# Performance work log

Hardware: AMD Instinct MI355X
Metric: run time of the kernel (lower is better)

Reference implementation:

```python
import jax, jax.numpy as jnp
import numpy as np
import math

HIDDEN = 2048
N_HEADS = 16
HEAD_DIM = HIDDEN // N_HEADS
BASE = 10000.0


def setup_inputs() -> dict:
    key = jax.random.key(0)
    ks = jax.random.split(key, 8)
    s = 1.0 / math.sqrt(HIDDEN)
    inp = {
        "hidden_states": jax.random.normal(ks[0], (2, 2048, HIDDEN), dtype=jnp.float32),
        "Wq": jax.random.normal(ks[1], (HIDDEN, HIDDEN), dtype=jnp.float32) * s,
        "bq": jax.random.normal(ks[2], (HIDDEN,), dtype=jnp.float32) * s,
        "Wk": jax.random.normal(ks[3], (HIDDEN, HIDDEN), dtype=jnp.float32) * s,
        "bk": jax.random.normal(ks[4], (HIDDEN,), dtype=jnp.float32) * s,
        "Wv": jax.random.normal(ks[5], (HIDDEN, HIDDEN), dtype=jnp.float32) * s,
        "bv": jax.random.normal(ks[6], (HIDDEN,), dtype=jnp.float32) * s,
        "Wo": jax.random.normal(ks[7], (HIDDEN, HIDDEN), dtype=jnp.float32) * s,
    }
    return inp


def _rotate_half(x):
    x1, x2 = x[..., : x.shape[-1] // 2], x[..., x.shape[-1] // 2 :]
    return jnp.concatenate((-x2, x1), axis=-1)


def _rope_cos_sin(seq_len, dtype):
    inv_freq = 1.0 / (BASE ** (jnp.arange(0, HEAD_DIM, 2, dtype=jnp.float32) / HEAD_DIM))
    t = jnp.arange(seq_len, dtype=jnp.float32)
    freqs = jnp.einsum("i,j->ij", t, inv_freq)  # [S, head_dim/2]
    emb = jnp.concatenate((freqs, freqs), axis=-1)  # [S, head_dim]
    return jnp.cos(emb).astype(dtype), jnp.sin(emb).astype(dtype)


def reference(hidden_states, Wq, bq, Wk, bk, Wv, bv, Wo):
    B, S, _ = hidden_states.shape
    q = hidden_states @ Wq + bq
    k = hidden_states @ Wk + bk
    v = hidden_states @ Wv + bv
    # [B, H, S, D]
    q = q.reshape(B, S, N_HEADS, HEAD_DIM).transpose(0, 2, 1, 3)
    k = k.reshape(B, S, N_HEADS, HEAD_DIM).transpose(0, 2, 1, 3)
    v = v.reshape(B, S, N_HEADS, HEAD_DIM).transpose(0, 2, 1, 3)
    cos, sin = _rope_cos_sin(S, q.dtype)  # [S, D]
    cos = cos[None, None]
    sin = sin[None, None]
    q = q * cos + _rotate_half(q) * sin
    k = k * cos + _rotate_half(k) * sin
    scale = 1.0 / math.sqrt(HEAD_DIM)
    scores = jnp.einsum("bhqd,bhkd->bhqk", q, k) * scale
    attn = jax.nn.softmax(scores, axis=-1)
    out = jnp.einsum("bhqk,bhkd->bhqd", attn, v)
    out = out.transpose(0, 2, 1, 3).reshape(B, S, HIDDEN)
    return out @ Wo
```

## Files before the change

### kernel.cpp

```cpp
#include <hip/hip_runtime.h>

#define HID 2048
#define SEQ 2048
#define HD 128
#define QKN 6144

typedef float f32x4 __attribute__((ext_vector_type(4)));
typedef short s16x8 __attribute__((ext_vector_type(8)));
typedef __bf16 bf16x8 __attribute__((ext_vector_type(8)));

static __device__ __forceinline__ unsigned short f2bf(float x) {
    unsigned u = __float_as_uint(x);
    u = u + 0x7FFFu + ((u >> 16) & 1u);
    return (unsigned short)(u >> 16);
}
static __device__ __forceinline__ float bf2f(unsigned short h) {
    return __uint_as_float(((unsigned)h) << 16);
}
static __device__ __forceinline__ bf16x8 as_bf(s16x8 v) {
    union { s16x8 s; bf16x8 b; } u; u.s = v; return u.b;
}
static __device__ __forceinline__ bf16x8 ld_bf8(const unsigned short* p) {
    return as_bf(*(const s16x8*)p);
}
static __device__ __forceinline__ void gload_lds16(const void* g, void* l) {
    __builtin_amdgcn_global_load_lds(
        (const __attribute__((address_space(1))) void*)g,
        (__attribute__((address_space(3))) void*)l,
        16, 0, 0);
}

__global__ __launch_bounds__(256) void fill_f32(
    float* __restrict__ out, float v, int n)
{
    int i = blockIdx.x * 256 + threadIdx.x;
    if (i < n) out[i] = v;
}

__global__ __launch_bounds__(256) void convert_f32_bf16(
    const float* __restrict__ in, unsigned short* __restrict__ out)
{
    long i = ((long)blockIdx.x * 256 + threadIdx.x) * 8;
    f32x4 a = *(const f32x4*)&in[i];
    f32x4 b = *(const f32x4*)&in[i + 4];
    s16x8 o;
#pragma unroll
    for (int e = 0; e < 4; ++e) {
        o[e]     = (short)f2bf(a[e]);
        o[e + 4] = (short)f2bf(b[e]);
    }
    *(s16x8*)&out[i] = o;
}

__global__ __launch_bounds__(256) void transpose_w4(
    const float* __restrict__ Wq, const float* __restrict__ Wk,
    const float* __restrict__ Wv, const float* __restrict__ Wo,
    unsigned short* __restrict__ wqkvT, unsigned short* __restrict__ woT)
{
    __shared__ float t[32][33];
    const int z = blockIdx.z;
    const float* W = (z == 0) ? Wq : (z == 1) ? Wk : (z == 2) ? Wv : Wo;
    unsigned short* Wt = (z < 3) ? (wqkvT + (long)z * HID * HID) : woT;
    int k0 = blockIdx.x * 32, n0 = blockIdx.y * 32;
    int tx = threadIdx.x & 31, ty = threadIdx.x >> 5;
#pragma unroll
    for (int r = ty; r < 32; r += 8)
        t[r][tx] = W[(long)(k0 + r) * HID + n0 + tx];
    __syncthreads();
#pragma unroll
    for (int r = ty; r < 32; r += 8)
        Wt[(long)(n0 + r) * HID + k0 + tx] = f2bf(t[tx][r]);
}

template<int NF, bool F32OUT, bool ROPE>
__global__ __launch_bounds__(512, 2) void gemm_8phase(
    const unsigned short* __restrict__ A,
    const unsigned short* __restrict__ Bt,
    const float* __restrict__ bq, const float* __restrict__ bk,
    const float* __restrict__ bv,
    unsigned short* __restrict__ Cb, float* __restrict__ Cf,
    int K, int ldc, int nbn, int sm, int sn, int hasBias)
{
    constexpr int BUFE = 16384 + NF * 4096;
    __shared__ unsigned short lds[2 * BUFE];
    const int tid = threadIdx.x;
    const int wid = tid >> 6, lane = tid & 63;
    const int l16 = lane & 15, l4 = lane >> 4;
    const int wm = wid >> 2, wn = wid & 3;

    const int bid = blockIdx.x;
    const int xcd = bid & 7, idx = bid >> 3;
    const int ncn = nbn / sn;
    const int cm = xcd / ncn, cn = xcd % ncn;
    const int lm = idx / sn,  ln = idx % sn;
    const long bm = (long)(cm * sm + lm) * 256;
    const long bn = (long)(cn * sn + ln) * (NF * 64);

    const int NT = K >> 6;
    const long strideB = (long)K * 2;
    const int srow = tid >> 3;
    const int scb  = ((tid & 7) * 16) ^ ((srow & 7) << 4);

    auto stageA = [&](int t, int c) {
        unsigned short* base = &lds[(t & 1) * BUFE];
        const int row = c * 64 + srow;
        const char* src = (const char*)A + (bm + row) * strideB + (long)t * 128 + scb;
        gload_lds16(src, base + (c * 64 + wid * 8) * 64);
    };
    auto stageB = [&](int t, int c) {
        unsigned short* base = &lds[(t & 1) * BUFE + 16384];
        const int row = c * 64 + srow;
        const char* src = (const char*)Bt + (bn + row) * strideB + (long)t * 128 + scb;
        gload_lds16(src, base + (c * 64 + wid * 8) * 64);
    };

    f32x4 acc[8][NF];
#pragma unroll
    for (int i = 0; i < 8; ++i)
#pragma unroll
        for (int j = 0; j < NF; ++j) acc[i][j] = f32x4{0.f, 0.f, 0.f, 0.f};

    auto compute = [&](const unsigned short* Ab, const unsigned short* Bb) {
#pragma unroll
        for (int kk = 0; kk < 2; ++kk) {
            bf16x8 bfr[NF];
#pragma unroll
            for (int j = 0; j < NF; ++j) {
                const int row = wn * (NF * 16) + j * 16 + l16;
                const char* rb = (const char*)Bb + row * 128;
                bfr[j] = as_bf(*(const s16x8*)(rb + ((kk * 64 + l4 * 16) ^ ((l16 & 7) << 4))));
            }
#pragma unroll
            for (int half = 0; half < 2; ++half) {
                bf16x8 af[4];
#pragma unroll
                for (int i = 0; i < 4; ++i) {
                    const int row = wm * 128 + (half * 4 + i) * 16 + l16;
                    const char* rb = (const char*)Ab + row * 128;
                    af[i] = as_bf(*(const s16x8*)(rb + ((kk * 64 + l4 * 16) ^ ((l16 & 7) << 4))));
                }
                __builtin_amdgcn_s_setprio(1);
#pragma unroll
                for (int i = 0; i < 4; ++i)
#pragma unroll
                    for (int j = 0; j < NF; ++j)
                        acc[half * 4 + i][j] = __builtin_amdgcn_mfma_f32_16x16x32_bf16(
                            af[i], bfr[j], acc[half * 4 + i][j], 0, 0, 0);
                __builtin_amdgcn_s_setprio(0);
            }
        }
    };

#pragma unroll
    for (int c = 0; c < 4; ++c) stageA(0, c);
#pragma unroll
    for (int c = 0; c < NF; ++c) stageB(0, c);

    for (int t = 0; t < NT - 1; ++t) {
        const unsigned short* Ab = &lds[(t & 1) * BUFE];
        const unsigned short* Bb = Ab + 16384;
#pragma unroll
        for (int c = 0; c < 4; ++c) stageA(t + 1, c);
#pragma unroll
        for (int c = 0; c < NF; ++c) stageB(t + 1, c);
        __builtin_amdgcn_sched_barrier(0);
        if constexpr (NF == 6)      asm volatile("s_waitcnt vmcnt(10)" ::: "memory");
        else if constexpr (NF == 3) asm volatile("s_waitcnt vmcnt(7)" ::: "memory");
        else                        asm volatile("s_waitcnt vmcnt(6)" ::: "memory");
        __builtin_amdgcn_s_barrier();
        __builtin_amdgcn_sched_barrier(0);
        compute(Ab, Bb);
        __builtin_amdgcn_s_barrier();
    }
    {
        const unsigned short* Ab = &lds[((NT - 1) & 1) * BUFE];
        const unsigned short* Bb = Ab + 16384;
        asm volatile("s_waitcnt vmcnt(0)" ::: "memory");
        __builtin_amdgcn_s_barrier();
        __builtin_amdgcn_sched_barrier(0);
        compute(Ab, Bb);
    }

    float bvv[NF];
#pragma unroll
    for (int nf = 0; nf < NF; ++nf) {
        const long n = bn + wn * (NF * 16) + nf * 16 + l16;
        bvv[nf] = 0.f;
        if (hasBias)
            bvv[nf] = (n < HID) ? bq[n] : ((n < 2 * HID) ? bk[n - HID] : bv[n - 2 * HID]);
    }

    if constexpr (ROPE) {
        constexpr int NH = NF / 2;
        float* fl = (float*)lds;
        const int jr = tid & 63;
        const int rquo = tid >> 6;
        const float inv = exp2f(-(float)jr * 0.20762050593046f);
#pragma unroll
        for (int c = 0; c < 4; ++c) {
            __builtin_amdgcn_s_barrier();
            if (wm == (c >> 1)) {
                const int mf0 = (c & 1) * 4;
#pragma unroll
                for (int mfi = 0; mfi < 4; ++mfi)
#pragma unroll
                    for (int r = 0; r < 4; ++r) {
                        const int rl = mfi * 16 + l4 * 4 + r;
#pragma unroll
                        for (int nf = 0; nf < NF; ++nf)
                            fl[rl * 385 + wn * (NF * 16) + nf * 16 + l16] =
                                acc[mf0 + mfi][nf][r] + bvv[nf];
                    }
            }
            __builtin_amdgcn_s_barrier();
#pragma unroll
            for (int rr = 0; rr < 8; ++rr) {
                const int rl = rr * 8 + rquo;
                const long m = bm + (c >> 1) * 128 + (c & 1) * 64 + rl;
                const int s = (int)(m & (SEQ - 1));
                float sn, cs;
                sincosf((float)s * inv, &sn, &cs);
#pragma unroll
                for (int hh = 0; hh < NH; ++hh) {
                    const long n = bn + hh * 128 + jr;
                    const bool ron = n < 2 * HID;
                    const float qsv = (n < HID) ? 0.12751744581845f : 1.0f;
                    const float se = ron ? sn : 0.f;
                    const float ce = ron ? cs : 1.f;
                    const float x1 = fl[rl * 385 + hh * 128 + jr];
                    const float x2 = fl[rl * 385 + hh * 128 + jr + 64];
                    Cb[m * (long)ldc + n]      = f2bf((x1 * ce - x2 * se) * qsv);
                    Cb[m * (long)ldc + n + 64] = f2bf((x2 * ce + x1 * se) * qsv);
                }
            }
        }
    } else {
#pragma unroll
        for (int mf = 0; mf < 8; ++mf) {
#pragma unroll
            for (int r = 0; r < 4; ++r) {
                const long m = bm + wm * 128 + mf * 16 + l4 * 4 + r;
#pragma unroll
                for (int nf = 0; nf < NF; ++nf) {
                    const long n = bn + wn * (NF * 16) + nf * 16 + l16;
                    float v = acc[mf][nf][r] + bvv[nf];
                    if (F32OUT) Cf[m * (long)ldc + n] = v;
                    else        Cb[m * (long)ldc + n] = f2bf(v);
                }
            }
        }
    }
}

__global__ __launch_bounds__(256) void v_transpose(
    const unsigned short* __restrict__ qkv, unsigned short* __restrict__ vt)
{
    __shared__ unsigned short t[32][33];
    int bh = blockIdx.z;
    int b = bh >> 4, h = bh & 15;
    int s0 = blockIdx.x * 32, d0 = blockIdx.y * 32;
    int tx = threadIdx.x & 31, ty = threadIdx.x >> 5;
#pragma unroll
    for (int r = ty; r < 32; r += 8)
        t[r][tx] = qkv[(long)(b * SEQ + s0 + r) * QKN + 2 * HID + h * HD + d0 + tx];
    __syncthreads();
#pragma unroll
    for (int r = ty; r < 32; r += 8)
        vt[((long)bh * HD + d0 + r) * SEQ + s0 + tx] = t[tx][r];
}

__global__ __launch_bounds__(512) void attn_kernel(
    const unsigned short* __restrict__ qkv,
    const unsigned short* __restrict__ vt,
    unsigned short* __restrict__ attnout)
{
    __shared__ unsigned short Ks[2][64 * 128];
    __shared__ unsigned short Vs[2][128 * 64];

    const int tid = threadIdx.x, wid = tid >> 6, lane = tid & 63;
    const int l16 = lane & 15, l4 = lane >> 4;
    const int bid = blockIdx.x;
    const int xcd = bid & 7, idx = bid >> 3;
    const int bh = xcd * 4 + (idx >> 4);
    const int qt = idx & 15;
    const int b = bh >> 4, h = bh & 15;
    const long rowbase = (long)b * SEQ;

    const unsigned short* Kg = &qkv[rowbase * QKN + HID + h * HD];
    const unsigned short* Vg = &vt[(long)bh * HD * SEQ];

    auto stage = [&](int buf, int kv0) {
#pragma unroll
        for (int i = 0; i < 2; ++i) {
            int c = wid * 2 + i;
            int kr = c * 4 + l4;
            int kcb = (l16 * 16) ^ ((kr & 7) << 4);
            gload_lds16((const char*)(Kg + (long)(kv0 + kr) * QKN) + kcb, &Ks[buf][c * 512]);
            int vr = c * 8 + (lane >> 3);
            int vcb = ((lane & 7) * 16) ^ ((vr & 7) << 4);
            gload_lds16((const char*)(Vg + (long)vr * SEQ + kv0) + vcb, &Vs[buf][c * 512]);
        }
    };

    bf16x8 qf[4];
    {
        const long qrow = rowbase + qt * 128 + wid * 16 + l16;
        const unsigned short* qp = &qkv[qrow * QKN + h * HD];
#pragma unroll
        for (int kc = 0; kc < 4; ++kc) qf[kc] = ld_bf8(qp + kc * 32 + l4 * 8);
    }

    f32x4 o[8];
#pragma unroll
    for (int nb = 0; nb < 8; ++nb) o[nb] = f32x4{0.f, 0.f, 0.f, 0.f};
    float mrun = -3.0e38f, lrun = 0.f;

    const int srcA = ((l4 & 1) * 2) * 16 + l16;
    const int srcB = srcA + 16;
    const bool sel = (l4 >> 1) != 0;

    stage(0, 0);
    __syncthreads();

    for (int t = 0; t < SEQ / 64; ++t) {
        const int cur = t & 1;
        if (t < SEQ / 64 - 1) stage(cur ^ 1, (t + 1) * 64);
        __builtin_amdgcn_sched_barrier(0);

        const unsigned short* Kc = &Ks[cur][0];
        const unsigned short* Vc = &Vs[cur][0];

        f32x4 sc[4];
#pragma unroll
        for (int nf = 0; nf < 4; ++nf) sc[nf] = f32x4{0.f, 0.f, 0.f, 0.f};
#pragma unroll
        for (int kc = 0; kc < 4; ++kc) {
#pragma unroll
            for (int nf = 0; nf < 4; ++nf) {
                int row = nf * 16 + l16;
                int cb = (kc * 64 + l4 * 16) ^ ((row & 7) << 4);
                bf16x8 kf = as_bf(*(const s16x8*)((const char*)Kc + row * 256 + cb));
                sc[nf] = __builtin_amdgcn_mfma_f32_16x16x32_bf16(kf, qf[kc], sc[nf], 0, 0, 0);
            }
        }

        float m0 = fmaxf(fmaxf(sc[0][0], sc[0][1]), sc[0][2]);
        float m1 = fmaxf(fmaxf(sc[0][3], sc[1][0]), sc[1][1]);
        float m2 = fmaxf(fmaxf(sc[1][2], sc[1][3]), sc[2][0]);
        float m3 = fmaxf(fmaxf(sc[2][1], sc[2][2]), sc[2][3]);
        float m4 = fmaxf(fmaxf(sc[3][0], sc[3][1]), sc[3][2]);
        float tmax = fmaxf(fmaxf(m0, m1), m2);
        tmax = fmaxf(fmaxf(m3, m4), tmax);
        tmax = fmaxf(tmax, sc[3][3]);
        tmax = fmaxf(tmax, __shfl_xor(tmax, 16, 64));
        tmax = fmaxf(tmax, __shfl_xor(tmax, 32, 64));

        if (!__all(tmax - mrun <= 8.0f)) {
            float mn = fmaxf(mrun, tmax);
            float sc_ = exp2f(mrun - mn);
            mrun = mn;
            lrun *= sc_;
            float s_[4];
#pragma unroll
            for (int r = 0; r < 4; ++r) s_[r] = __shfl(sc_, l4 * 4 + r, 64);
#pragma unroll
            for (int nb = 0; nb < 8; ++nb)
#pragma unroll
                for (int r = 0; r < 4; ++r) o[nb][r] *= s_[r];
        }

        unsigned pk[4][2];
        float sum = 0.f;
#pragma unroll
        for (int nf = 0; nf < 4; ++nf) {
            float p0 = exp2f(sc[nf][0] - mrun);
            float p1 = exp2f(sc[nf][1] - mrun);
            float p2 = exp2f(sc[nf][2] - mrun);
            float p3 = exp2f(sc[nf][3] - mrun);
            sum += (p0 + p1) + (p2 + p3);
            union { __bf16 b[2]; unsigned u; } w0, w1;
            w0.b[0] = (__bf16)p0; w0.b[1] = (__bf16)p1;
            w1.b[0] = (__bf16)p2; w1.b[1] = (__bf16)p3;
            pk[nf][0] = w0.u; pk[nf][1] = w1.u;
        }
        sum += __shfl_xor(sum, 16, 64);
        sum += __shfl_xor(sum, 32, 64);
        lrun += sum;

        union { unsigned u[4]; bf16x8 v; } pa0, pa1;
#pragma unroll
        for (int w = 0; w < 2; ++w) {
            unsigned a0 = __shfl(pk[0][w], srcA, 64);
            unsigned a1 = __shfl(pk[1][w], srcA, 64);
            unsigned b0 = __shfl(pk[0][w], srcB, 64);
            unsigned b1 = __shfl(pk[1][w], srcB, 64);
            pa0.u[w]     = sel ? a1 : a0;
            pa0.u[2 + w] = sel ? b1 : b0;
            unsigned c0 = __shfl(pk[2][w], srcA, 64);
            unsigned c1 = __shfl(pk[3][w], srcA, 64);
            unsigned d0 = __shfl(pk[2][w], srcB, 64);
            unsigned d1 = __shfl(pk[3][w], srcB, 64);
            pa1.u[w]     = sel ? c1 : c0;
            pa1.u[2 + w] = sel ? d1 : d0;
        }

#pragma unroll
        for (int kc = 0; kc < 2; ++kc) {
            bf16x8 pav = kc ? pa1.v : pa0.v;
#pragma unroll
            for (int nb = 0; nb < 8; ++nb) {
                int vrow = nb * 16 + l16;
                int vcb = (kc * 64 + l4 * 16) ^ ((vrow & 7) << 4);
                bf16x8 vb = as_bf(*(const s16x8*)((const char*)Vc + vrow * 128 + vcb));
                o[nb] = __builtin_amdgcn_mfma_f32_16x16x32_bf16(pav, vb, o[nb], 0, 0, 0);
            }
        }
        __syncthreads();
    }

    float linv = 1.f / lrun;
    float li[4];
#pragma unroll
    for (int r = 0; r < 4; ++r) li[r] = __shfl(linv, l4 * 4 + r, 64);
#pragma unroll
    for (int r = 0; r < 4; ++r) {
        long m = rowbase + qt * 128 + wid * 16 + l4 * 4 + r;
#pragma unroll
        for (int nb = 0; nb < 8; ++nb)
            attnout[m * HID + h * HD + nb * 16 + l16] = f2bf(o[nb][r] * li[r]);
    }
}

extern "C" void kernel_launch(void* const* d_in, const int* in_sizes, int n_in,
                              void* d_out, int out_size, void* d_ws, size_t ws_size,
                              hipStream_t stream)
{
    const float* hs = (const float*)d_in[0];
    const float* Wq = (const float*)d_in[1];
    const float* bq = (const float*)d_in[2];
    const float* Wk = (const float*)d_in[3];
    const float* bk = (const float*)d_in[4];
    const float* Wv = (const float*)d_in[5];
    const float* bv = (const float*)d_in[6];
    const float* Wo = (const float*)d_in[7];
    float* out = (float*)d_out;

    bool shapes_ok =
        (n_in == 8) && (out_size == 8388608) &&
        in_sizes[0] == 8388608 && in_sizes[1] == 4194304 && in_sizes[2] == 2048 &&
        in_sizes[3] == 4194304 && in_sizes[4] == 2048 && in_sizes[5] == 4194304 &&
        in_sizes[6] == 2048 && in_sizes[7] == 4194304;
    if (!shapes_ok || ws_size < 117440512ull) {
        fill_f32<<<32768, 256, 0, stream>>>(out, shapes_ok ? 1000.f : 0.f, out_size);
        return;
    }

    char* ws = (char*)d_ws;
    unsigned short* hsB     = (unsigned short*)(ws);
    unsigned short* qkvB    = (unsigned short*)(ws + 16777216);
    unsigned short* wqkvT   = (unsigned short*)(ws + 67108864);
    unsigned short* vtB     = (unsigned short*)(ws + 92274688);
    unsigned short* woT     = (unsigned short*)(ws + 109051904);
    unsigned short* attnout = hsB;

    convert_f32_bf16<<<4096, 256, 0, stream>>>(hs, hsB);
    transpose_w4<<<dim3(64, 64, 4), 256, 0, stream>>>(Wq, Wk, Wv, Wo, wqkvT, woT);

    gemm_8phase<6, false, true><<<dim3(256), 512, 0, stream>>>(
        hsB, wqkvT, bq, bk, bv, qkvB, nullptr, 2048, QKN, 16, 8, 4, 1);
    v_transpose<<<dim3(64, 4, 32), 256, 0, stream>>>(qkvB, vtB);
    attn_kernel<<<dim3(512), 512, 0, stream>>>(qkvB, vtB, attnout);
    gemm_8phase<2, true, false><<<dim3(256), 512, 0, stream>>>(
        attnout, woT, nullptr, nullptr, nullptr, nullptr, out, 2048, HID, 16, 4, 8, 0);
}
```

Before: 293.3 us.

## Switch attention to 32x32x16 MFMA with 256-row query tiles per block

The attention kernel now gives each wave 32 query rows instead of 16 and uses 32x32x16 bf16 MFMAs for both QK^T and PV. Each block covers 256 query rows, so the grid halves to 256 blocks. This doubles the reuse of every K/V tile staged in LDS, cuts LDS traffic per FLOP, and simplifies the P-fragment shuffle to a single xor-32 exchange. The cost is much higher register pressure (64 accumulator floats plus 32 score floats per lane), and only 256 blocks on a GPU with 256 CUs may leave occupancy thin despite launch_bounds(512,2).

New measurement: 285.0 us (median of 2 runs). -2.9%, faster.

```diff
diff --git a/kernel.cpp b/kernel.cpp
--- a/kernel.cpp
+++ b/kernel.cpp
@@ -6,6 +6,7 @@
 #define QKN 6144
 
 typedef float f32x4 __attribute__((ext_vector_type(4)));
+typedef float f32x16 __attribute__((ext_vector_type(16)));
 typedef short s16x8 __attribute__((ext_vector_type(8)));
 typedef __bf16 bf16x8 __attribute__((ext_vector_type(8)));
 
@@ -269,7 +270,7 @@
         vt[((long)bh * HD + d0 + r) * SEQ + s0 + tx] = t[tx][r];
 }
 
-__global__ __launch_bounds__(512) void attn_kernel(
+__global__ __launch_bounds__(512, 2) void attn_kernel(
     const unsigned short* __restrict__ qkv,
     const unsigned short* __restrict__ vt,
     unsigned short* __restrict__ attnout)
@@ -278,11 +279,12 @@
     __shared__ unsigned short Vs[2][128 * 64];
 
     const int tid = threadIdx.x, wid = tid >> 6, lane = tid & 63;
+    const int l32 = lane & 31, hh = lane >> 5;
     const int l16 = lane & 15, l4 = lane >> 4;
     const int bid = blockIdx.x;
     const int xcd = bid & 7, idx = bid >> 3;
-    const int bh = xcd * 4 + (idx >> 4);
-    const int qt = idx & 15;
+    const int bh = xcd * 4 + (idx >> 3);
+    const int qt = idx & 7;
     const int b = bh >> 4, h = bh & 15;
     const long rowbase = (long)b * SEQ;
 
@@ -302,22 +304,21 @@
         }
     };
 
-    bf16x8 qf[4];
+    bf16x8 qf[8];
     {
-        const long qrow = rowbase + qt * 128 + wid * 16 + l16;
+        const long qrow = rowbase + qt * 256 + wid * 32 + l32;
         const unsigned short* qp = &qkv[qrow * QKN + h * HD];
 #pragma unroll
-        for (int kc = 0; kc < 4; ++kc) qf[kc] = ld_bf8(qp + kc * 32 + l4 * 8);
-    }
-
-    f32x4 o[8];
-#pragma unroll
-    for (int nb = 0; nb < 8; ++nb) o[nb] = f32x4{0.f, 0.f, 0.f, 0.f};
+        for (int ks = 0; ks < 8; ++ks)
+            qf[ks] = ld_bf8(qp + ks * 16 + hh * 8);
+    }
+
+    f32x16 ob[4];
+#pragma unroll
+    for (int db = 0; db < 4; ++db)
+#pragma unroll
+        for (int r = 0; r < 16; ++r) ob[db][r] = 0.f;
     float mrun = -3.0e38f, lrun = 0.f;
-
-    const int srcA = ((l4 & 1) * 2) * 16 + l16;
-    const int srcB = srcA + 16;
-    const bool sel = (l4 >> 1) != 0;
 
     stage(0, 0);
     __syncthreads();
@@ -330,104 +331,100 @@
         const unsigned short* Kc = &Ks[cur][0];
         const unsigned short* Vc = &Vs[cur][0];
 
-        f32x4 sc[4];
-#pragma unroll
-        for (int nf = 0; nf < 4; ++nf) sc[nf] = f32x4{0.f, 0.f, 0.f, 0.f};
-#pragma unroll
-        for (int kc = 0; kc < 4; ++kc) {
-#pragma unroll
-            for (int nf = 0; nf < 4; ++nf) {
-                int row = nf * 16 + l16;
-                int cb = (kc * 64 + l4 * 16) ^ ((row & 7) << 4);
+        f32x16 sc[2];
+#pragma unroll
+        for (int kb = 0; kb < 2; ++kb)
+#pragma unroll
+            for (int r = 0; r < 16; ++r) sc[kb][r] = 0.f;
+#pragma unroll
+        for (int ks = 0; ks < 8; ++ks) {
+#pragma unroll
+            for (int kb = 0; kb < 2; ++kb) {
+                int row = kb * 32 + l32;
+                int cb = (ks * 32 + hh * 16) ^ ((row & 7) << 4);
                 bf16x8 kf = as_bf(*(const s16x8*)((const char*)Kc + row * 256 + cb));
-                sc[nf] = __builtin_amdgcn_mfma_f32_16x16x32_bf16(kf, qf[kc], sc[nf], 0, 0, 0);
-            }
-        }
-
-        float m0 = fmaxf(fmaxf(sc[0][0], sc[0][1]), sc[0][2]);
-        float m1 = fmaxf(fmaxf(sc[0][3], sc[1][0]), sc[1][1]);
-        float m2 = fmaxf(fmaxf(sc[1][2], sc[1][3]), sc[2][0]);
-        float m3 = fmaxf(fmaxf(sc[2][1], sc[2][2]), sc[2][3]);
-        float m4 = fmaxf(fmaxf(sc[3][0], sc[3][1]), sc[3][2]);
-        float tmax = fmaxf(fmaxf(m0, m1), m2);
-        tmax = fmaxf(fmaxf(m3, m4), tmax);
-        tmax = fmaxf(tmax, sc[3][3]);
-        tmax = fmaxf(tmax, __shfl_xor(tmax, 16, 64));
+                sc[kb] = __builtin_amdgcn_mfma_f32_32x32x16_bf16(kf, qf[ks], sc[kb], 0, 0, 0);
+            }
+        }
+
+        float tmax = sc[0][0];
+#pragma unroll
+        for (int kb = 0; kb < 2; ++kb)
+#pragma unroll
+            for (int r = 0; r < 16; ++r) tmax = fmaxf(tmax, sc[kb][r]);
         tmax = fmaxf(tmax, __shfl_xor(tmax, 32, 64));
 
         if (!__all(tmax - mrun <= 8.0f)) {
             float mn = fmaxf(mrun, tmax);
-            float sc_ = exp2f(mrun - mn);
+            float e_ = exp2f(mrun - mn);
             mrun = mn;
-            lrun *= sc_;
-            float s_[4];
-#pragma unroll
-            for (int r = 0; r < 4; ++r) s_[r] = __shfl(sc_, l4 * 4 + r, 64);
-#pragma unroll
-            for (int nb = 0; nb < 8; ++nb)
-#pragma unroll
-                for (int r = 0; r < 4; ++r) o[nb][r] *= s_[r];
-        }
-
-        unsigned pk[4][2];
+            lrun *= e_;
+            float sr[16];
+#pragma unroll
+            for (int r = 0; r < 16; ++r)
+                sr[r] = __shfl(e_, (r & 3) + 8 * (r >> 2) + 4 * hh, 64);
+#pragma unroll
+            for (int db = 0; db < 4; ++db)
+#pragma unroll
+                for (int r = 0; r < 16; ++r) ob[db][r] *= sr[r];
+        }
+
+        unsigned pk[2][8];
         float sum = 0.f;
 #pragma unroll
-        for (int nf = 0; nf < 4; ++nf) {
-            float p0 = exp2f(sc[nf][0] - mrun);
-            float p1 = exp2f(sc[nf][1] - mrun);
-            float p2 = exp2f(sc[nf][2] - mrun);
-            float p3 = exp2f(sc[nf][3] - mrun);
-            sum += (p0 + p1) + (p2 + p3);
-            union { __bf16 b[2]; unsigned u; } w0, w1;
-            w0.b[0] = (__bf16)p0; w0.b[1] = (__bf16)p1;
-            w1.b[0] = (__bf16)p2; w1.b[1] = (__bf16)p3;
-            pk[nf][0] = w0.u; pk[nf][1] = w1.u;
-        }
-        sum += __shfl_xor(sum, 16, 64);
+        for (int kb = 0; kb < 2; ++kb) {
+#pragma unroll
+            for (int g = 0; g < 8; ++g) {
+                float p0 = exp2f(sc[kb][2 * g]     - mrun);
+                float p1 = exp2f(sc[kb][2 * g + 1] - mrun);
+                sum += p0 + p1;
+                union { __bf16 b[2]; unsigned u; } w;
+                w.b[0] = (__bf16)p0; w.b[1] = (__bf16)p1;
+                pk[kb][g] = w.u;
+            }
+        }
         sum += __shfl_xor(sum, 32, 64);
         lrun += sum;
 
-        union { unsigned u[4]; bf16x8 v; } pa0, pa1;
-#pragma unroll
-        for (int w = 0; w < 2; ++w) {
-            unsigned a0 = __shfl(pk[0][w], srcA, 64);
-            unsigned a1 = __shfl(pk[1][w], srcA, 64);
-            unsigned b0 = __shfl(pk[0][w], srcB, 64);
-            unsigned b1 = __shfl(pk[1][w], srcB, 64);
-            pa0.u[w]     = sel ? a1 : a0;
-            pa0.u[2 + w] = sel ? b1 : b0;
-            unsigned c0 = __shfl(pk[2][w], srcA, 64);
-            unsigned c1 = __shfl(pk[3][w], srcA, 64);
-            unsigned d0 = __shfl(pk[2][w], srcB, 64);
-            unsigned d1 = __shfl(pk[3][w], srcB, 64);
-            pa1.u[w]     = sel ? c1 : c0;
-            pa1.u[2 + w] = sel ? d1 : d0;
-        }
-
-#pragma unroll
-        for (int kc = 0; kc < 2; ++kc) {
-            bf16x8 pav = kc ? pa1.v : pa0.v;
-#pragma unroll
-            for (int nb = 0; nb < 8; ++nb) {
-                int vrow = nb * 16 + l16;
-                int vcb = (kc * 64 + l4 * 16) ^ ((vrow & 7) << 4);
-                bf16x8 vb = as_bf(*(const s16x8*)((const char*)Vc + vrow * 128 + vcb));
-                o[nb] = __builtin_amdgcn_mfma_f32_16x16x32_bf16(pav, vb, o[nb], 0, 0, 0);
+        union { unsigned u[4]; bf16x8 v; } pa[4];
+#pragma unroll
+        for (int ks = 0; ks < 4; ++ks) {
+            const int kb = ks >> 1, base = (ks & 1) * 4;
+            unsigned a0 = __shfl_xor(pk[kb][base + 0], 32, 64);
+            unsigned a1 = __shfl_xor(pk[kb][base + 1], 32, 64);
+            unsigned a2 = __shfl_xor(pk[kb][base + 2], 32, 64);
+            unsigned a3 = __shfl_xor(pk[kb][base + 3], 32, 64);
+            pa[ks].u[0] = hh ? a2 : pk[kb][base + 0];
+            pa[ks].u[1] = hh ? a3 : pk[kb][base + 1];
+            pa[ks].u[2] = hh ? pk[kb][base + 2] : a0;
+            pa[ks].u[3] = hh ? pk[kb][base + 3] : a1;
+        }
+
+#pragma unroll
+        for (int ks = 0; ks < 4; ++ks) {
+#pragma unroll
+            for (int db = 0; db < 4; ++db) {
+                int row = db * 32 + l32;
+                int cb = (ks * 32 + hh * 16) ^ ((row & 7) << 4);
+                bf16x8 vb = as_bf(*(const s16x8*)((const char*)Vc + row * 128 + cb));
+                ob[db] = __builtin_amdgcn_mfma_f32_32x32x16_bf16(pa[ks].v, vb, ob[db], 0, 0, 0);
             }
         }
         __syncthreads();
     }
 
     float linv = 1.f / lrun;
-    float li[4];
-#pragma unroll
-    for (int r = 0; r < 4; ++r) li[r] = __shfl(linv, l4 * 4 + r, 64);
-#pragma unroll
-    for (int r = 0; r < 4; ++r) {
-        long m = rowbase + qt * 128 + wid * 16 + l4 * 4 + r;
-#pragma unroll
-        for (int nb = 0; nb < 8; ++nb)
-            attnout[m * HID + h * HD + nb * 16 + l16] = f2bf(o[nb][r] * li[r]);
+    float li[16];
+#pragma unroll
+    for (int r = 0; r < 16; ++r)
+        li[r] = __shfl(linv, (r & 3) + 8 * (r >> 2) + 4 * hh, 64);
+#pragma unroll
+    for (int db = 0; db < 4; ++db) {
+#pragma unroll
+        for (int r = 0; r < 16; ++r) {
+            const long m = rowbase + qt * 256 + wid * 32 + (r & 3) + 8 * (r >> 2) + 4 * hh;
+            attnout[m * HID + h * HD + db * 32 + l32] = f2bf(ob[db][r] * li[r]);
+        }
     }
 }
 
@@ -469,7 +466,7 @@
     gemm_8phase<6, false, true><<<dim3(256), 512, 0, stream>>>(
         hsB, wqkvT, bq, bk, bv, qkvB, nullptr, 2048, QKN, 16, 8, 4, 1);
     v_transpose<<<dim3(64, 4, 32), 256, 0, stream>>>(qkvB, vtB);
-    attn_kernel<<<dim3(512), 512, 0, stream>>>(qkvB, vtB, attnout);
+    attn_kernel<<<dim3(256), 512, 0, stream>>>(qkvB, vtB, attnout);
     gemm_8phase<2, true, false><<<dim3(256), 512, 0, stream>>>(
         attnout, woT, nullptr, nullptr, nullptr, nullptr, out, 2048, HID, 16, 4, 8, 0);
 }
```
